# Kernel tuning notes

Measured on AMD Instinct MI355X. Metric: run time of the kernel, lower is better.

The kernel has to match this reference:

```python
import jax, jax.numpy as jnp
import numpy as np

NX = NY = NZ = 192
DX = DY = DZ = 1e-3
DT = 1e-12
EPS0 = 8.8541878128e-12
MU0 = 1.25663706212e-6


def _dcentral(f, axis, inv2d):
    # central difference along `axis`, defined only on the interior of ALL
    # three dims (matches the torch edge lists built for i,j,k in 1..n-2);
    # boundary entries are zero (no scatter contributions there).
    g = jnp.zeros_like(f)
    sp = [slice(1, -1)] * 3
    sm = [slice(1, -1)] * 3
    sp[axis] = slice(2, None)
    sm[axis] = slice(0, -2)
    return g.at[1:-1, 1:-1, 1:-1].set((f[tuple(sp)] - f[tuple(sm)]) * inv2d)


def setup_inputs() -> dict:
    key = jax.random.key(0)
    ks = jax.random.split(key, 9)
    shp = (1, 1, NX, NY, NZ)
    f32 = jnp.float32
    inp = {}
    for name, k in zip(['Ex', 'Ey', 'Ez', 'Hx', 'Hy', 'Hz'], ks[:6]):
        inp[name] = jax.random.normal(k, shp, dtype=f32)
    inp['eps'] = (EPS0 * (1.0 + jax.random.uniform(ks[6], shp))).astype(f32)
    inp['mu'] = (MU0 * (1.0 + jax.random.uniform(ks[7], shp))).astype(f32)
    inp['sigma'] = (1e-3 * jax.random.uniform(ks[8], shp)).astype(f32)
    return inp


def reference(Ex, Ey, Ez, Hx, Hy, Hz, eps, mu, sigma):
    inv2dx = 1.0 / (2.0 * DX)
    inv2dy = 1.0 / (2.0 * DY)
    inv2dz = 1.0 / (2.0 * DZ)
    r3 = lambda a: a.reshape(NX, NY, NZ)  # _flatten3 equivalent layout
    ex, ey, ez = r3(Ex), r3(Ey), r3(Ez)
    hx, hy, hz = r3(Hx), r3(Hy), r3(Hz)
    eps3, mu3, sig3 = r3(eps), r3(mu), r3(sigma)

    # Step 1 (E -> H): H^{n+1/2} = H^{n-1/2} - dt/mu * curl(E^n)
    curlE_x = _dcentral(ez, 1, inv2dy) - _dcentral(ey, 2, inv2dz)
    curlE_y = _dcentral(ex, 2, inv2dz) - _dcentral(ez, 0, inv2dx)
    curlE_z = _dcentral(ey, 0, inv2dx) - _dcentral(ex, 1, inv2dy)
    hx2 = hx - (DT / mu3) * curlE_x
    hy2 = hy - (DT / mu3) * curlE_y
    hz2 = hz - (DT / mu3) * curlE_z

    # Step 2 (H -> E): E^{n+1} = (A-/A+) E^n + dt/(eps A+) * curl(H^{n+1/2})
    A_plus = 1.0 + sig3 * DT / (2.0 * eps3)
    A_minus = 1.0 - sig3 * DT / (2.0 * eps3)
    curlH_x = _dcentral(hz2, 1, inv2dy) - _dcentral(hy2, 2, inv2dz)
    curlH_y = _dcentral(hx2, 2, inv2dz) - _dcentral(hz2, 0, inv2dx)
    curlH_z = _dcentral(hy2, 0, inv2dx) - _dcentral(hx2, 1, inv2dy)
    coefE = A_minus / A_plus
    coefC = DT / (eps3 * A_plus)
    ex2 = coefE * ex + coefC * curlH_x
    ey2 = coefE * ey + coefC * curlH_y
    ez2 = coefE * ez + coefC * curlH_z

    u5 = lambda a: a.reshape(1, 1, NX, NY, NZ)  # _unflatten3
    return (u5(ex2), u5(ey2), u5(ez2), u5(hx2), u5(hy2), u5(hz2))
```

## Files before the change

### kernel.cpp

```cpp
#include <hip/hip_runtime.h>


#define NXD 192
#define NYD 192
#define NZD 192

static constexpr int   N3    = NXD * NYD * NZD;
static constexpr float DTc   = 1e-12f;
static constexpr float INV2D = 500.0f;

static constexpr int TX = 8, TY = 8, TZ = 32;
static constexpr int HXT = 10, HYT = 10;
static constexpr int ZCH = 10;
static constexpr int ZSTR = 40;
static constexpr int LVOL = HXT * HYT * ZSTR;
static constexpr int NCH  = HXT * HYT * ZCH;
static constexpr int NBX = NXD / TX, NBY = NYD / TY, NBZ = NZD / TZ;
static constexpr int NBLK = NBX * NBY * NBZ;

__device__ __forceinline__ int clampi(int v, int lo, int hi) {
    return v < lo ? lo : (v > hi ? hi : v);
}

__global__ __launch_bounds__(256, 3) void fdtd_fused(
    const float* __restrict__ Ex, const float* __restrict__ Ey, const float* __restrict__ Ez,
    const float* __restrict__ Hx, const float* __restrict__ Hy, const float* __restrict__ Hz,
    const float* __restrict__ eps, const float* __restrict__ mu, const float* __restrict__ sigma,
    float* __restrict__ Ex2, float* __restrict__ Ey2, float* __restrict__ Ez2,
    float* __restrict__ Hx2, float* __restrict__ Hy2, float* __restrict__ Hz2)
{
    __shared__ float sHx[LVOL];
    __shared__ float sHy[LVOL];
    __shared__ float sHz[LVOL];

    int bid = blockIdx.x;
    int swz = (bid & 7) * (NBLK / 8) + (bid >> 3);
    int bz = swz % NBZ;
    int t0 = swz / NBZ;
    int by = t0 % NBY;
    int bx = t0 / NBY;
    int ox = bx * TX, oy = by * TY, oz = bz * TZ;

    int tid = threadIdx.x;

    for (int it = 0; it < 4; ++it) {
        int h = tid + it * 256;
        if (h < NCH) {
            int cz = h % ZCH;
            int tt = h / ZCH;
            int hy = tt % HYT;
            int hx = tt / HYT;

            int gi = ox + hx - 1;
            int gj = oy + hy - 1;
            int kb = oz + cz * 4 - 4;

            int gic  = clampi(gi,     0, NXD - 1);
            int gjc  = clampi(gj,     0, NYD - 1);
            int gipc = clampi(gi + 1, 0, NXD - 1);
            int gimc = clampi(gi - 1, 0, NXD - 1);
            int gjpc = clampi(gj + 1, 0, NYD - 1);
            int gjmc = clampi(gj - 1, 0, NYD - 1);
            int kbc  = clampi(kb,     0, NZD - 4);
            int km1  = clampi(kb - 1, 0, NZD - 1);
            int kp4  = clampi(kb + 4, 0, NZD - 1);

            int rowC  = (gic  * NYD + gjc ) * NZD;
            int rowXp = (gipc * NYD + gjc ) * NZD;
            int rowXm = (gimc * NYD + gjc ) * NZD;
            int rowYp = (gic  * NYD + gjpc) * NZD;
            int rowYm = (gic  * NYD + gjmc) * NZD;

            float4 ezYp = *(const float4*)(Ez + rowYp + kbc);
            float4 ezYm = *(const float4*)(Ez + rowYm + kbc);
            float4 exYp = *(const float4*)(Ex + rowYp + kbc);
            float4 exYm = *(const float4*)(Ex + rowYm + kbc);
            float4 eyXp = *(const float4*)(Ey + rowXp + kbc);
            float4 eyXm = *(const float4*)(Ey + rowXm + kbc);
            float4 ezXp = *(const float4*)(Ez + rowXp + kbc);
            float4 ezXm = *(const float4*)(Ez + rowXm + kbc);
            float4 eyC  = *(const float4*)(Ey + rowC + kbc);
            float4 exC  = *(const float4*)(Ex + rowC + kbc);
            float  ey_m1 = Ey[rowC + km1], ey_p4 = Ey[rowC + kp4];
            float  ex_m1 = Ex[rowC + km1], ex_p4 = Ex[rowC + kp4];
            float4 hxC = *(const float4*)(Hx + rowC + kbc);
            float4 hyC = *(const float4*)(Hy + rowC + kbc);
            float4 hzC = *(const float4*)(Hz + rowC + kbc);
            float4 muC = *(const float4*)(mu + rowC + kbc);

            const float* ezYpf = (const float*)&ezYp; const float* ezYmf = (const float*)&ezYm;
            const float* exYpf = (const float*)&exYp; const float* exYmf = (const float*)&exYm;
            const float* eyXpf = (const float*)&eyXp; const float* eyXmf = (const float*)&eyXm;
            const float* ezXpf = (const float*)&ezXp; const float* ezXmf = (const float*)&ezXm;
            const float* eyCf  = (const float*)&eyC;  const float* exCf  = (const float*)&exC;
            const float* hxCf  = (const float*)&hxC;  const float* hyCf  = (const float*)&hyC;
            const float* hzCf  = (const float*)&hzC;  const float* muCf  = (const float*)&muC;

            float4 vx, vy, vz;
            float* vxf = (float*)&vx; float* vyf = (float*)&vy; float* vzf = (float*)&vz;

            bool xyok = (gi >= 1) && (gi <= NXD - 2) && (gj >= 1) && (gj <= NYD - 2);
            #pragma unroll
            for (int e = 0; e < 4; ++e) {
                int ke = kb + e;
                bool valid = xyok && (ke >= 1) && (ke <= NZD - 2);
                float eyzm = (e == 0) ? ey_m1 : eyCf[e - 1];
                float eyzp = (e == 3) ? ey_p4 : eyCf[e + 1];
                float exzm = (e == 0) ? ex_m1 : exCf[e - 1];
                float exzp = (e == 3) ? ex_p4 : exCf[e + 1];
                float cx = valid ? ((ezYpf[e] - ezYmf[e]) - (eyzp - eyzm)) * INV2D : 0.0f;
                float cy = valid ? ((exzp - exzm) - (ezXpf[e] - ezXmf[e])) * INV2D : 0.0f;
                float cc = valid ? ((eyXpf[e] - eyXmf[e]) - (exYpf[e] - exYmf[e])) * INV2D : 0.0f;
                float f = DTc / muCf[e];
                vxf[e] = hxCf[e] - f * cx;
                vyf[e] = hyCf[e] - f * cy;
                vzf[e] = hzCf[e] - f * cc;
            }

            int l = (hx * HYT + hy) * ZSTR + cz * 4;
            *(float4*)(sHx + l) = vx;
            *(float4*)(sHy + l) = vy;
            *(float4*)(sHz + l) = vz;

            if (hx >= 1 && hx <= TX && hy >= 1 && hy <= TY && cz >= 1 && cz <= 8) {
                int gidx = rowC + kb;
                *(float4*)(Hx2 + gidx) = vx;
                *(float4*)(Hy2 + gidx) = vy;
                *(float4*)(Hz2 + gidx) = vz;
            }
        }
    }

    __syncthreads();

    for (int it = 0; it < 2; ++it) {
        int c  = tid + it * 256;
        int zc = c & 7;
        int tt = c >> 3;
        int iy = tt & 7;
        int ix = tt >> 3;
        int gi = ox + ix, gj = oy + iy;
        int k0 = oz + zc * 4;
        int gidx = (gi * NYD + gj) * NZD + k0;
        int l0 = ((ix + 1) * HYT + (iy + 1)) * ZSTR + zc * 4 + 4;

        float4 hzYp = *(const float4*)(sHz + l0 + ZSTR);
        float4 hzYm = *(const float4*)(sHz + l0 - ZSTR);
        float4 hxYp = *(const float4*)(sHx + l0 + ZSTR);
        float4 hxYm = *(const float4*)(sHx + l0 - ZSTR);
        float4 hzXp = *(const float4*)(sHz + l0 + HYT * ZSTR);
        float4 hzXm = *(const float4*)(sHz + l0 - HYT * ZSTR);
        float4 hyXp = *(const float4*)(sHy + l0 + HYT * ZSTR);
        float4 hyXm = *(const float4*)(sHy + l0 - HYT * ZSTR);
        float4 hyCv = *(const float4*)(sHy + l0);
        float4 hxCv = *(const float4*)(sHx + l0);
        float  hy_m1 = sHy[l0 - 1], hy_p4 = sHy[l0 + 4];
        float  hx_m1 = sHx[l0 - 1], hx_p4 = sHx[l0 + 4];

        float4 exC  = *(const float4*)(Ex + gidx);
        float4 eyC  = *(const float4*)(Ey + gidx);
        float4 ezC  = *(const float4*)(Ez + gidx);
        float4 epsC = *(const float4*)(eps + gidx);
        float4 sigC = *(const float4*)(sigma + gidx);

        const float* hzYpf = (const float*)&hzYp; const float* hzYmf = (const float*)&hzYm;
        const float* hxYpf = (const float*)&hxYp; const float* hxYmf = (const float*)&hxYm;
        const float* hzXpf = (const float*)&hzXp; const float* hzXmf = (const float*)&hzXm;
        const float* hyXpf = (const float*)&hyXp; const float* hyXmf = (const float*)&hyXm;
        const float* hyCf  = (const float*)&hyCv; const float* hxCf  = (const float*)&hxCv;
        const float* exCf  = (const float*)&exC;  const float* eyCf  = (const float*)&eyC;
        const float* ezCf  = (const float*)&ezC;
        const float* epsf  = (const float*)&epsC; const float* sigf  = (const float*)&sigC;

        float4 ex2, ey2, ez2;
        float* ex2f = (float*)&ex2; float* ey2f = (float*)&ey2; float* ez2f = (float*)&ez2;

        bool xyok = (gi >= 1) && (gi <= NXD - 2) && (gj >= 1) && (gj <= NYD - 2);
        #pragma unroll
        for (int e = 0; e < 4; ++e) {
            int ke = k0 + e;
            bool valid = xyok && (ke >= 1) && (ke <= NZD - 2);
            float hyzm = (e == 0) ? hy_m1 : hyCf[e - 1];
            float hyzp = (e == 3) ? hy_p4 : hyCf[e + 1];
            float hxzm = (e == 0) ? hx_m1 : hxCf[e - 1];
            float hxzp = (e == 3) ? hx_p4 : hxCf[e + 1];
            float cx = valid ? ((hzYpf[e] - hzYmf[e]) - (hyzp - hyzm)) * INV2D : 0.0f;
            float cy = valid ? ((hxzp - hxzm) - (hzXpf[e] - hzXmf[e])) * INV2D : 0.0f;
            float cc = valid ? ((hyXpf[e] - hyXmf[e]) - (hxYpf[e] - hxYmf[e])) * INV2D : 0.0f;

            float ee = epsf[e];
            float ss = sigf[e];
            float half_sdt_over_e = ss * DTc / (2.0f * ee);
            float Ap = 1.0f + half_sdt_over_e;
            float Am = 1.0f - half_sdt_over_e;
            float coefE = Am / Ap;
            float coefC = DTc / (ee * Ap);
            ex2f[e] = coefE * exCf[e] + coefC * cx;
            ey2f[e] = coefE * eyCf[e] + coefC * cy;
            ez2f[e] = coefE * ezCf[e] + coefC * cc;
        }

        *(float4*)(Ex2 + gidx) = ex2;
        *(float4*)(Ey2 + gidx) = ey2;
        *(float4*)(Ez2 + gidx) = ez2;
    }
}

extern "C" void kernel_launch(void* const* d_in, const int* in_sizes, int n_in,
                              void* d_out, int out_size, void* d_ws, size_t ws_size,
                              hipStream_t stream)
{
    const float* Ex    = (const float*)d_in[0];
    const float* Ey    = (const float*)d_in[1];
    const float* Ez    = (const float*)d_in[2];
    const float* Hx    = (const float*)d_in[3];
    const float* Hy    = (const float*)d_in[4];
    const float* Hz    = (const float*)d_in[5];
    const float* eps   = (const float*)d_in[6];
    const float* mu    = (const float*)d_in[7];
    const float* sigma = (const float*)d_in[8];

    float* out = (float*)d_out;
    float* Ex2 = out + 0 * (size_t)N3;
    float* Ey2 = out + 1 * (size_t)N3;
    float* Ez2 = out + 2 * (size_t)N3;
    float* Hx2 = out + 3 * (size_t)N3;
    float* Hy2 = out + 4 * (size_t)N3;
    float* Hz2 = out + 5 * (size_t)N3;

    fdtd_fused<<<NBLK, 256, 0, stream>>>(Ex, Ey, Ez, Hx, Hy, Hz, eps, mu, sigma,
                                         Ex2, Ey2, Ez2, Hx2, Hy2, Hz2);
}
```

Before: 442.0 us.

## Halve z-tile and store only needed halo per H component in LDS

```diff
diff --git a/kernel.cpp b/kernel.cpp
--- a/kernel.cpp
+++ b/kernel.cpp
@@ -9,12 +9,15 @@
 static constexpr float DTc   = 1e-12f;
 static constexpr float INV2D = 500.0f;
 
-static constexpr int TX = 8, TY = 8, TZ = 32;
+static constexpr int TX = 8, TY = 8, TZ = 16;
 static constexpr int HXT = 10, HYT = 10;
-static constexpr int ZCH = 10;
-static constexpr int ZSTR = 40;
-static constexpr int LVOL = HXT * HYT * ZSTR;
-static constexpr int NCH  = HXT * HYT * ZCH;
+static constexpr int ZCH = 6;
+static constexpr int NCH = HXT * HYT * ZCH;
+
+static constexpr int SHX_X = 280, SHX_Y = 28;
+static constexpr int SHY_X = 224, SHY_Y = 28;
+static constexpr int SHZ_X = 200, SHZ_Y = 20;
+
 static constexpr int NBX = NXD / TX, NBY = NYD / TY, NBZ = NZD / TZ;
 static constexpr int NBLK = NBX * NBY * NBZ;
 
@@ -22,16 +25,16 @@
     return v < lo ? lo : (v > hi ? hi : v);
 }
 
-__global__ __launch_bounds__(256, 3) void fdtd_fused(
+__global__ __launch_bounds__(256, 6) void fdtd_fused(
     const float* __restrict__ Ex, const float* __restrict__ Ey, const float* __restrict__ Ez,
     const float* __restrict__ Hx, const float* __restrict__ Hy, const float* __restrict__ Hz,
     const float* __restrict__ eps, const float* __restrict__ mu, const float* __restrict__ sigma,
     float* __restrict__ Ex2, float* __restrict__ Ey2, float* __restrict__ Ez2,
     float* __restrict__ Hx2, float* __restrict__ Hy2, float* __restrict__ Hz2)
 {
-    __shared__ float sHx[LVOL];
-    __shared__ float sHy[LVOL];
-    __shared__ float sHz[LVOL];
+    __shared__ float sHx[8 * 10 * 28];
+    __shared__ float sHy[10 * 8 * 28];
+    __shared__ float sHz[10 * 10 * 20];
 
     int bid = blockIdx.x;
     int swz = (bid & 7) * (NBLK / 8) + (bid >> 3);
@@ -43,7 +46,8 @@
 
     int tid = threadIdx.x;
 
-    for (int it = 0; it < 4; ++it) {
+    #pragma unroll
+    for (int it = 0; it < 3; ++it) {
         int h = tid + it * 256;
         if (h < NCH) {
             int cz = h % ZCH;
@@ -117,12 +121,14 @@
                 vzf[e] = hzCf[e] - f * cc;
             }
 
-            int l = (hx * HYT + hy) * ZSTR + cz * 4;
-            *(float4*)(sHx + l) = vx;
-            *(float4*)(sHy + l) = vy;
-            *(float4*)(sHz + l) = vz;
-
-            if (hx >= 1 && hx <= TX && hy >= 1 && hy <= TY && cz >= 1 && cz <= 8) {
+            if (hx >= 1 && hx <= 8)
+                *(float4*)(sHx + (hx - 1) * SHX_X + hy * SHX_Y + cz * 4) = vx;
+            if (hy >= 1 && hy <= 8)
+                *(float4*)(sHy + hx * SHY_X + (hy - 1) * SHY_Y + cz * 4) = vy;
+            if (cz >= 1 && cz <= 4)
+                *(float4*)(sHz + hx * SHZ_X + hy * SHZ_Y + (cz - 1) * 4) = vz;
+
+            if (hx >= 1 && hx <= 8 && hy >= 1 && hy <= 8 && cz >= 1 && cz <= 4) {
                 int gidx = rowC + kb;
                 *(float4*)(Hx2 + gidx) = vx;
                 *(float4*)(Hy2 + gidx) = vy;
@@ -133,29 +139,13 @@
 
     __syncthreads();
 
-    for (int it = 0; it < 2; ++it) {
-        int c  = tid + it * 256;
-        int zc = c & 7;
-        int tt = c >> 3;
-        int iy = tt & 7;
-        int ix = tt >> 3;
+    {
+        int zc = tid & 3;
+        int iy = (tid >> 2) & 7;
+        int ix = tid >> 5;
         int gi = ox + ix, gj = oy + iy;
         int k0 = oz + zc * 4;
         int gidx = (gi * NYD + gj) * NZD + k0;
-        int l0 = ((ix + 1) * HYT + (iy + 1)) * ZSTR + zc * 4 + 4;
-
-        float4 hzYp = *(const float4*)(sHz + l0 + ZSTR);
-        float4 hzYm = *(const float4*)(sHz + l0 - ZSTR);
-        float4 hxYp = *(const float4*)(sHx + l0 + ZSTR);
-        float4 hxYm = *(const float4*)(sHx + l0 - ZSTR);
-        float4 hzXp = *(const float4*)(sHz + l0 + HYT * ZSTR);
-        float4 hzXm = *(const float4*)(sHz + l0 - HYT * ZSTR);
-        float4 hyXp = *(const float4*)(sHy + l0 + HYT * ZSTR);
-        float4 hyXm = *(const float4*)(sHy + l0 - HYT * ZSTR);
-        float4 hyCv = *(const float4*)(sHy + l0);
-        float4 hxCv = *(const float4*)(sHx + l0);
-        float  hy_m1 = sHy[l0 - 1], hy_p4 = sHy[l0 + 4];
-        float  hx_m1 = sHx[l0 - 1], hx_p4 = sHx[l0 + 4];
 
         float4 exC  = *(const float4*)(Ex + gidx);
         float4 eyC  = *(const float4*)(Ey + gidx);
@@ -163,9 +153,26 @@
         float4 epsC = *(const float4*)(eps + gidx);
         float4 sigC = *(const float4*)(sigma + gidx);
 
+        int lx = ix * SHX_X + (iy + 1) * SHX_Y + zc * 4 + 4;
+        int ly = (ix + 1) * SHY_X + iy * SHY_Y + zc * 4 + 4;
+        int lz = (ix + 1) * SHZ_X + (iy + 1) * SHZ_Y + zc * 4;
+
+        float4 hzYp = *(const float4*)(sHz + lz + SHZ_Y);
+        float4 hzYm = *(const float4*)(sHz + lz - SHZ_Y);
+        float4 hzXp = *(const float4*)(sHz + lz + SHZ_X);
+        float4 hzXm = *(const float4*)(sHz + lz - SHZ_X);
+        float4 hxYp = *(const float4*)(sHx + lx + SHX_Y);
+        float4 hxYm = *(const float4*)(sHx + lx - SHX_Y);
+        float4 hyXp = *(const float4*)(sHy + ly + SHY_X);
+        float4 hyXm = *(const float4*)(sHy + ly - SHY_X);
+        float4 hyCv = *(const float4*)(sHy + ly);
+        float4 hxCv = *(const float4*)(sHx + lx);
+        float  hy_m1 = sHy[ly - 1], hy_p4 = sHy[ly + 4];
+        float  hx_m1 = sHx[lx - 1], hx_p4 = sHx[lx + 4];
+
         const float* hzYpf = (const float*)&hzYp; const float* hzYmf = (const float*)&hzYm;
+        const float* hzXpf = (const float*)&hzXp; const float* hzXmf = (const float*)&hzXm;
         const float* hxYpf = (const float*)&hxYp; const float* hxYmf = (const float*)&hxYm;
-        const float* hzXpf = (const float*)&hzXp; const float* hzXmf = (const float*)&hzXm;
         const float* hyXpf = (const float*)&hyXp; const float* hyXmf = (const float*)&hyXm;
         const float* hyCf  = (const float*)&hyCv; const float* hxCf  = (const float*)&hxCv;
         const float* exCf  = (const float*)&exC;  const float* eyCf  = (const float*)&eyC;
```

Measured after the change: 486.8 us. 10.2% more time.
